# Optimization experiments

Hardware: AMD Instinct MI355X
Metric: run time of the kernel (lower is better)

## Reference

```python
import jax, jax.numpy as jnp
import numpy as np

M, K, N = 8192, 4096, 4096
EPS = 1e-7


def setup_inputs() -> dict:
    key = jax.random.key(0)
    k1, k2, k3 = jax.random.split(key, 3)
    x = jax.random.normal(k1, (M, K), dtype=jnp.float32)
    # Build a float weight and quantize per output channel (per_channel_quant)
    w = jax.random.normal(k2, (N, K), dtype=jnp.float32)
    absmax = jnp.max(jnp.abs(w), axis=1, keepdims=True)          # [N,1]
    w_scale = absmax / 127.0                                      # fp32 per-channel scale
    weight_q = jnp.clip(jnp.round(w / w_scale), -128, 127).astype(jnp.int8)
    bias = (jax.random.normal(k3, (N,), dtype=jnp.float32) * 0.02).astype(jnp.float16)
    return {"x": x, "weight_q": weight_q, "w_scale": w_scale, "bias": bias}


def reference(x, weight_q, w_scale, bias):
    # per_token_quant_int8: dynamic per-token scale = absmax/127 (eps-clamped)
    absmax = jnp.max(jnp.abs(x), axis=-1, keepdims=True)          # [M,1]
    x_scale = jnp.maximum(absmax, EPS) / 127.0
    x_q = jnp.clip(jnp.round(x / x_scale), -128, 127).astype(jnp.int8)
    acc = jnp.matmul(x_q.astype(jnp.int32), weight_q.astype(jnp.int32).T)  # [M,N] int32
    # dequant: per-token scale * per-channel scale, add bias, cast fp16
    out = acc.astype(jnp.float32) * x_scale * w_scale.reshape(1, -1)
    out = out + bias.astype(jnp.float32)
    return out.astype(jnp.float16)
```

## Files before the change

### kernel.cpp

```cpp
#include <hip/hip_runtime.h>
#include <hip/hip_fp16.h>
#include <cstdint>
#include <cstddef>


#define MDIM 8192
#define KDIM 4096
#define NDIM 4096

typedef int v4i  __attribute__((ext_vector_type(4)));
typedef int v16i __attribute__((ext_vector_type(16)));

__device__ __forceinline__ void load_lds_16(const void* g, void* l) {
  __builtin_amdgcn_global_load_lds((const __attribute__((address_space(1))) void*)g,
                                   (__attribute__((address_space(3))) void*)l,
                                   16, 0, 0);
}

extern "C" __global__ __launch_bounds__(256)
void qlin_quant_x(const float* __restrict__ x, int8_t* __restrict__ xq,
                  float* __restrict__ xs) {
  const int row = blockIdx.x;
  const int t   = threadIdx.x;
  const float4* xr = (const float4*)(x + (size_t)row * KDIM);
  float4 v[4];
  float amax = 0.f;
#pragma unroll
  for (int i = 0; i < 4; ++i) {
    v[i] = xr[t + 256 * i];
    amax = fmaxf(amax, fmaxf(fmaxf(fabsf(v[i].x), fabsf(v[i].y)),
                             fmaxf(fabsf(v[i].z), fabsf(v[i].w))));
  }
#pragma unroll
  for (int off = 32; off > 0; off >>= 1)
    amax = fmaxf(amax, __shfl_xor(amax, off, 64));
  __shared__ float smax[4];
  if ((t & 63) == 0) smax[t >> 6] = amax;
  __syncthreads();
  amax = fmaxf(fmaxf(smax[0], smax[1]), fmaxf(smax[2], smax[3]));
  const float scale = fmaxf(amax, 1e-7f) / 127.0f;
  if (t == 0) xs[row] = scale;
  int* outp = (int*)(xq + (size_t)row * KDIM);
#pragma unroll
  for (int i = 0; i < 4; ++i) {
    int q0 = (int)rintf(v[i].x / scale);
    int q1 = (int)rintf(v[i].y / scale);
    int q2 = (int)rintf(v[i].z / scale);
    int q3 = (int)rintf(v[i].w / scale);
    q0 = min(127, max(-128, q0));
    q1 = min(127, max(-128, q1));
    q2 = min(127, max(-128, q2));
    q3 = min(127, max(-128, q3));
    outp[t + 256 * i] = (q0 & 0xff) | ((q1 & 0xff) << 8) |
                        ((q2 & 0xff) << 16) | ((q3 & 0xff) << 24);
  }
}

extern "C" __global__ __launch_bounds__(256)
void qlin_pack_w(const int* __restrict__ w32, int8_t* __restrict__ w8) {
  const int idx = blockIdx.x * 256 + threadIdx.x;
  const int4 w = ((const int4*)w32)[idx];
  ((int*)w8)[idx] = (w.x & 0xff) | ((w.y & 0xff) << 8) |
                    ((w.z & 0xff) << 16) | ((w.w & 0xff) << 24);
}

extern "C" __global__ __launch_bounds__(256)
void qlin_gemm(const int8_t* __restrict__ Aq, const int8_t* __restrict__ Bq,
               const float* __restrict__ xs, const float* __restrict__ ws,
               const float* __restrict__ bias, float* __restrict__ out) {
  __shared__ int8_t As[128 * 64];
  __shared__ int8_t Bs[128 * 64];
  const int tid  = threadIdx.x;
  const int lane = tid & 63;
  const int wave = tid >> 6;
  const int wr   = wave >> 1;
  const int wc   = wave & 1;
  const int m0   = blockIdx.y * 128;
  const int n0   = blockIdx.x * 128;

  const int srow = tid >> 2;
  const int scol = (tid & 3) * 16;

  const int8_t* Ab = Aq + (size_t)m0 * KDIM;
  const int8_t* Bb = Bq + (size_t)n0 * KDIM;

  v16i acc[2][2];
#pragma unroll
  for (int i = 0; i < 2; ++i)
#pragma unroll
    for (int j = 0; j < 2; ++j)
#pragma unroll
      for (int r = 0; r < 16; ++r) acc[i][j][r] = 0;

  const int r = lane & 31;
  const int g = (lane >> 5) * 16;

  for (int k0 = 0; k0 < KDIM; k0 += 64) {
    load_lds_16(Ab + (size_t)srow * KDIM + (k0 + scol), As + tid * 16);
    load_lds_16(Ab + (size_t)(srow + 64) * KDIM + (k0 + scol), As + 4096 + tid * 16);
    load_lds_16(Bb + (size_t)srow * KDIM + (k0 + scol), Bs + tid * 16);
    load_lds_16(Bb + (size_t)(srow + 64) * KDIM + (k0 + scol), Bs + 4096 + tid * 16);
    __builtin_amdgcn_s_waitcnt(0);
    __syncthreads();

#pragma unroll
    for (int ks = 0; ks < 2; ++ks) {
      v4i a[2], b[2];
#pragma unroll
      for (int i = 0; i < 2; ++i)
        a[i] = *(const v4i*)(As + (wr * 64 + i * 32 + r) * 64 + ks * 32 + g);
#pragma unroll
      for (int j = 0; j < 2; ++j)
        b[j] = *(const v4i*)(Bs + (wc * 64 + j * 32 + r) * 64 + ks * 32 + g);
#pragma unroll
      for (int i = 0; i < 2; ++i)
#pragma unroll
        for (int j = 0; j < 2; ++j)
          acc[i][j] = __builtin_amdgcn_mfma_i32_32x32x32_i8(a[i], b[j], acc[i][j], 0, 0, 0);
    }
    __syncthreads();
  }

  const int col = lane & 31;
  const int rb  = (lane >> 5) * 4;
#pragma unroll
  for (int j = 0; j < 2; ++j) {
    const int gc = n0 + wc * 64 + j * 32 + col;
    const float wsv = ws[gc];
    const float bv  = bias[gc];
#pragma unroll
    for (int i = 0; i < 2; ++i) {
      const int grb = m0 + wr * 64 + i * 32 + rb;
#pragma unroll
      for (int reg = 0; reg < 16; ++reg) {
        const int gr = grb + (reg & 3) + 8 * (reg >> 2);
        float t = (float)acc[i][j][reg] * xs[gr];
        t = t * wsv + bv;
        out[(size_t)gr * NDIM + gc] = __half2float(__float2half(t));
      }
    }
  }
}

extern "C" void kernel_launch(void* const* d_in, const int* in_sizes, int n_in,
                              void* d_out, int out_size, void* d_ws, size_t ws_size,
                              hipStream_t stream) {
  const float* x      = (const float*)d_in[0];
  const int*   wq32   = (const int*)d_in[1];
  const float* wscale = (const float*)d_in[2];
  const float* bias   = (const float*)d_in[3];
  float*       out    = (float*)d_out;

  int8_t* xq = (int8_t*)d_ws;
  int8_t* w8 = (int8_t*)d_ws + (size_t)MDIM * KDIM;
  float*  xs = (float*)((int8_t*)d_ws + (size_t)MDIM * KDIM + (size_t)NDIM * KDIM);

  qlin_quant_x<<<MDIM, 256, 0, stream>>>(x, xq, xs);
  qlin_pack_w<<<(NDIM * KDIM / 4) / 256, 256, 0, stream>>>(wq32, w8);
  qlin_gemm<<<dim3(NDIM / 128, MDIM / 128), 256, 0, stream>>>(xq, w8, xs, wscale, bias, out);
}
```

Baseline: 437.9 us.

## Double-buffer GEMM with BK=128, XOR-swizzled LDS, tile swizzle, merged prep kernel

The GEMM now uses double-buffered LDS with BK=128 and prefetches the next tile with global_load_lds while computing on the current one. It drops the explicit waitcnt and XOR-swizzles the LDS layout to avoid bank conflicts on the MFMA operand reads. Blocks are remapped through a 1D grid swizzle to improve L2 reuse. The x-quant and weight-pack kernels are merged into one launch, and the division is replaced by a reciprocal multiply. The LDS footprint rises to 64KB per block, and the missing waitcnt before the barrier may let the next iteration read LDS before the async loads have landed.

Result: no change. 440.9 us (+0.7%).

```diff
diff --git a/kernel.cpp b/kernel.cpp
--- a/kernel.cpp
+++ b/kernel.cpp
@@ -7,6 +7,11 @@
 #define MDIM 8192
 #define KDIM 4096
 #define NDIM 4096
+
+#define BM 128
+#define BN 128
+#define BK 128
+#define NT (KDIM / BK)
 
 typedef int v4i  __attribute__((ext_vector_type(4)));
 typedef int v16i __attribute__((ext_vector_type(16)));
@@ -18,10 +23,18 @@
 }
 
 extern "C" __global__ __launch_bounds__(256)
-void qlin_quant_x(const float* __restrict__ x, int8_t* __restrict__ xq,
-                  float* __restrict__ xs) {
+void qlin_prep(const float* __restrict__ x, int8_t* __restrict__ xq,
+               float* __restrict__ xs, const int* __restrict__ w32,
+               int8_t* __restrict__ w8) {
+  const int t = threadIdx.x;
+  if (blockIdx.x >= MDIM) {
+    const size_t idx = (size_t)(blockIdx.x - MDIM) * 256 + t;
+    const int4 w = ((const int4*)w32)[idx];
+    ((int*)w8)[idx] = (w.x & 0xff) | ((w.y & 0xff) << 8) |
+                      ((w.z & 0xff) << 16) | ((w.w & 0xff) << 24);
+    return;
+  }
   const int row = blockIdx.x;
-  const int t   = threadIdx.x;
   const float4* xr = (const float4*)(x + (size_t)row * KDIM);
   float4 v[4];
   float amax = 0.f;
@@ -39,14 +52,15 @@
   __syncthreads();
   amax = fmaxf(fmaxf(smax[0], smax[1]), fmaxf(smax[2], smax[3]));
   const float scale = fmaxf(amax, 1e-7f) / 127.0f;
+  const float inv   = 1.0f / scale;
   if (t == 0) xs[row] = scale;
   int* outp = (int*)(xq + (size_t)row * KDIM);
 #pragma unroll
   for (int i = 0; i < 4; ++i) {
-    int q0 = (int)rintf(v[i].x / scale);
-    int q1 = (int)rintf(v[i].y / scale);
-    int q2 = (int)rintf(v[i].z / scale);
-    int q3 = (int)rintf(v[i].w / scale);
+    int q0 = (int)rintf(v[i].x * inv);
+    int q1 = (int)rintf(v[i].y * inv);
+    int q2 = (int)rintf(v[i].z * inv);
+    int q3 = (int)rintf(v[i].w * inv);
     q0 = min(127, max(-128, q0));
     q1 = min(127, max(-128, q1));
     q2 = min(127, max(-128, q2));
@@ -56,33 +70,51 @@
   }
 }
 
-extern "C" __global__ __launch_bounds__(256)
-void qlin_pack_w(const int* __restrict__ w32, int8_t* __restrict__ w8) {
-  const int idx = blockIdx.x * 256 + threadIdx.x;
-  const int4 w = ((const int4*)w32)[idx];
-  ((int*)w8)[idx] = (w.x & 0xff) | ((w.y & 0xff) << 8) |
-                    ((w.z & 0xff) << 16) | ((w.w & 0xff) << 24);
-}
-
-extern "C" __global__ __launch_bounds__(256)
+extern "C" __global__ __launch_bounds__(256, 2)
 void qlin_gemm(const int8_t* __restrict__ Aq, const int8_t* __restrict__ Bq,
                const float* __restrict__ xs, const float* __restrict__ ws,
                const float* __restrict__ bias, float* __restrict__ out) {
-  __shared__ int8_t As[128 * 64];
-  __shared__ int8_t Bs[128 * 64];
+  __shared__ int8_t As[2][BM * BK];
+  __shared__ int8_t Bs[2][BN * BK];
   const int tid  = threadIdx.x;
   const int lane = tid & 63;
   const int wave = tid >> 6;
   const int wr   = wave >> 1;
   const int wc   = wave & 1;
-  const int m0   = blockIdx.y * 128;
-  const int n0   = blockIdx.x * 128;
 
-  const int srow = tid >> 2;
-  const int scol = (tid & 3) * 16;
+  const int id  = blockIdx.x;
+  const int swz = (id & 7) * 256 + (id >> 3);
+  const int bx  = swz & 31;
+  const int by  = swz >> 5;
+  const int m0  = by * BM;
+  const int n0  = bx * BN;
 
   const int8_t* Ab = Aq + (size_t)m0 * KDIM;
   const int8_t* Bb = Bq + (size_t)n0 * KDIM;
+
+  int srow[4], scsw[4], sdst[4];
+#pragma unroll
+  for (int it = 0; it < 4; ++it) {
+    const int q = (wave * 4 + it) * 64 + lane;
+    const int rr = q >> 3;
+    const int c  = q & 7;
+    srow[it] = rr;
+    scsw[it] = ((c ^ (rr & 7)) << 4);
+    sdst[it] = q * 16;
+  }
+
+  const int r  = lane & 31;
+  const int hi = lane >> 5;
+  const int rx = r & 7;
+  int aoff[2][4], boff[2][4];
+#pragma unroll
+  for (int i = 0; i < 2; ++i)
+#pragma unroll
+    for (int ks = 0; ks < 4; ++ks) {
+      const int kphys = ((ks * 2 + hi) ^ rx) << 4;
+      aoff[i][ks] = (wr * 64 + i * 32 + r) * BK + kphys;
+      boff[i][ks] = (wc * 64 + i * 32 + r) * BK + kphys;
+    }
 
   v16i acc[2][2];
 #pragma unroll
@@ -90,28 +122,29 @@
 #pragma unroll
     for (int j = 0; j < 2; ++j)
 #pragma unroll
-      for (int r = 0; r < 16; ++r) acc[i][j][r] = 0;
+      for (int rg = 0; rg < 16; ++rg) acc[i][j][rg] = 0;
 
-  const int r = lane & 31;
-  const int g = (lane >> 5) * 16;
+  auto STAGE = [&](int k0, int buf) {
+#pragma unroll
+    for (int it = 0; it < 4; ++it) {
+      load_lds_16(Ab + (size_t)srow[it] * KDIM + (k0 + scsw[it]), &As[buf][sdst[it]]);
+      load_lds_16(Bb + (size_t)srow[it] * KDIM + (k0 + scsw[it]), &Bs[buf][sdst[it]]);
+    }
+  };
 
-  for (int k0 = 0; k0 < KDIM; k0 += 64) {
-    load_lds_16(Ab + (size_t)srow * KDIM + (k0 + scol), As + tid * 16);
-    load_lds_16(Ab + (size_t)(srow + 64) * KDIM + (k0 + scol), As + 4096 + tid * 16);
-    load_lds_16(Bb + (size_t)srow * KDIM + (k0 + scol), Bs + tid * 16);
-    load_lds_16(Bb + (size_t)(srow + 64) * KDIM + (k0 + scol), Bs + 4096 + tid * 16);
-    __builtin_amdgcn_s_waitcnt(0);
-    __syncthreads();
+  STAGE(0, 0);
+  __syncthreads();
 
+  int buf = 0;
+  for (int t = 0; t < NT; ++t) {
+    if (t + 1 < NT) STAGE((t + 1) * BK, buf ^ 1);
 #pragma unroll
-    for (int ks = 0; ks < 2; ++ks) {
+    for (int ks = 0; ks < 4; ++ks) {
       v4i a[2], b[2];
 #pragma unroll
-      for (int i = 0; i < 2; ++i)
-        a[i] = *(const v4i*)(As + (wr * 64 + i * 32 + r) * 64 + ks * 32 + g);
+      for (int i = 0; i < 2; ++i) a[i] = *(const v4i*)(&As[buf][aoff[i][ks]]);
 #pragma unroll
-      for (int j = 0; j < 2; ++j)
-        b[j] = *(const v4i*)(Bs + (wc * 64 + j * 32 + r) * 64 + ks * 32 + g);
+      for (int j = 0; j < 2; ++j) b[j] = *(const v4i*)(&Bs[buf][boff[j][ks]]);
 #pragma unroll
       for (int i = 0; i < 2; ++i)
 #pragma unroll
@@ -119,10 +152,11 @@
           acc[i][j] = __builtin_amdgcn_mfma_i32_32x32x32_i8(a[i], b[j], acc[i][j], 0, 0, 0);
     }
     __syncthreads();
+    buf ^= 1;
   }
 
   const int col = lane & 31;
-  const int rb  = (lane >> 5) * 4;
+  const int rb  = hi * 4;
 #pragma unroll
   for (int j = 0; j < 2; ++j) {
     const int gc = n0 + wc * 64 + j * 32 + col;
@@ -134,9 +168,9 @@
 #pragma unroll
       for (int reg = 0; reg < 16; ++reg) {
         const int gr = grb + (reg & 3) + 8 * (reg >> 2);
-        float t = (float)acc[i][j][reg] * xs[gr];
-        t = t * wsv + bv;
-        out[(size_t)gr * NDIM + gc] = __half2float(__float2half(t));
+        float t2 = (float)acc[i][j][reg] * xs[gr];
+        t2 = t2 * wsv + bv;
+        out[(size_t)gr * NDIM + gc] = __half2float(__float2half(t2));
       }
     }
   }
@@ -155,7 +189,6 @@
   int8_t* w8 = (int8_t*)d_ws + (size_t)MDIM * KDIM;
   float*  xs = (float*)((int8_t*)d_ws + (size_t)MDIM * KDIM + (size_t)NDIM * KDIM);
 
-  qlin_quant_x<<<MDIM, 256, 0, stream>>>(x, xq, xs);
-  qlin_pack_w<<<(NDIM * KDIM / 4) / 256, 256, 0, stream>>>(wq32, w8);
-  qlin_gemm<<<dim3(NDIM / 128, MDIM / 128), 256, 0, stream>>>(xq, w8, xs, wscale, bias, out);
+  qlin_prep<<<MDIM + (NDIM * KDIM / 4) / 256, 256, 0, stream>>>(x, xq, xs, wq32, w8);
+  qlin_gemm<<<(MDIM / BM) * (NDIM / BN), 256, 0, stream>>>(xq, w8, xs, wscale, bias, out);
 }
```
